# Kernel tuning notes

Hardware: AMD Instinct MI355X
Metric: run time of the kernel (lower is better)

Reference implementation:

```python
import math
import jax, jax.numpy as jnp
from jax import lax
import numpy as np

TWO_PI = 2.0 * math.pi
CG_ITERS = 30      # DifferentiableLinearSolver(max_iter=30)
CG_TOL = 1e-6
CG_REG = 1e-6      # reg = 1e-6 * I added inside the solver


def build_second_diff_matrix(N, dtype):
    e = jnp.ones(N, dtype)
    e2 = -2.0 * e
    e2 = e2.at[0].set(-1.0).at[-1].set(-1.0)
    oper = jnp.diag(e2) + jnp.diag(e[:-1], -1) + jnp.diag(e[:-1], 1)
    return oper.T @ oper


def cumtrapz(y, dx):
    # cumulative trapezoid along last axis, keeping length (leading zero)
    avg = (y[..., :-1] + y[..., 1:]) * (0.5 * dx)
    c = jnp.cumsum(avg, axis=-1)
    return jnp.concatenate([jnp.zeros_like(y[..., :1]), c], axis=-1)


def differ5(y, delta):
    mid = (y[..., 2:] - y[..., :-2]) / (2.0 * delta)
    first = (y[..., 1:2] - y[..., 0:1]) / delta
    last = (y[..., -1:] - y[..., -2:-1]) / delta
    return jnp.concatenate([first, mid, last], axis=-1)


def projec5(vec, var):
    # per-row norm-ball projection; vec: (B, N)
    M = vec.shape[-1]
    e = jnp.sqrt(M * var)
    n = jnp.linalg.norm(vec, axis=-1, keepdims=True)
    scale = jnp.where(n > e, e / jnp.maximum(n, 1e-30), 1.0)
    return vec * scale


def cg_solve(opedoub, coef, diagv, rhs, x0):
    # Solves (coef*opedoub + diag(diagv) + CG_REG*I) x = rhs via CG,
    # matching torch semantics (early break freezes state).
    def mv(p):
        return coef * (opedoub @ p) + (diagv + CG_REG) * p

    r0 = rhs - mv(x0)
    rs0 = jnp.dot(r0, r0)

    def step(carry, _):
        x, r, p, rsold, done = carry
        Ap = mv(p)
        a = rsold / (jnp.dot(p, Ap) + 1e-12)
        x1 = jnp.where(done, x, x + a * p)
        r1 = jnp.where(done, r, r - a * Ap)
        rsnew = jnp.dot(r1, r1)
        done1 = done | (jnp.sqrt(rsnew) < CG_TOL)
        bta = rsnew / (rsold + 1e-12)
        p1 = jnp.where(done1, p, r1 + bta * p)
        rsold1 = jnp.where(done1, rsold, rsnew)
        return (x1, r1, p1, rsold1, done1), None

    (x, _, _, _, _), _ = lax.scan(step, (x0, r0, r0, rs0, jnp.array(False)), None, length=CG_ITERS)
    return x


def _forward(s, eIF, xm, ym, sum_x, sum_y, lamuda, init_freqs, mode_mask,
             alpha, beta, var, fs, iteration,
             fe_w1, fe_b1, fe_w2, fe_b2,
             pr_w1, pr_b1, pr_w2, pr_b2, pr_w3, pr_b3, iter_weight):
    dtype = s.dtype
    B, N = s.shape
    K = eIF.shape[1]

    # ---- hyperparameter refinement MLP ----
    avg = jnp.mean(init_freqs, axis=1, keepdims=True)              # (B,1)
    h = jax.nn.relu(avg @ fe_w1.T + fe_b1)
    h = jax.nn.relu(h @ fe_w2.T + fe_b2)                            # (B,16)
    cur = jnp.stack([jnp.broadcast_to(alpha, (B,)),
                     jnp.broadcast_to(beta, (B,))], axis=1)         # (B,2)
    z = jnp.concatenate([h, cur], axis=1)                           # (B,18)
    z = jax.nn.relu(z @ pr_w1.T + pr_b1)
    z = jax.nn.relu(z @ pr_w2.T + pr_b2)
    res = jnp.tanh(z @ pr_w3.T + pr_b3)                             # (B,2)
    fac = jax.nn.sigmoid(iter_weight * iteration)
    res = res * fac * 0.1
    new_alpha = jnp.clip(alpha + jnp.mean(res[:, 0] * alpha), 1e-6, 0.01)
    new_beta = jnp.clip(beta + jnp.mean(res[:, 1] * beta), 1e-6, 0.1)

    betathr = jnp.minimum(10.0 ** (iteration / 36.0 - 10.0), new_beta)
    opedoub = build_second_diff_matrix(N, dtype)
    dx = 1.0 / fs

    # Within the torch k-loop, temp sums / lamuda / new_eIF[b,k] all still hold
    # their *input* values, so all (b,k) sub-problems are independent -> vmap.
    u = projec5(s - sum_x - sum_y - lamuda / new_alpha, var)        # (B,N)

    phase = TWO_PI * cumtrapz(eIF, dx)                               # (B,K,N)
    cosm = jnp.cos(phase)
    sinm = jnp.sin(phase)
    resid = (s[:, None, :] - (sum_x[:, None, :] - xm * cosm)
             - (sum_y[:, None, :] - ym * sinm)
             - u[:, None, :] - (lamuda / new_alpha)[:, None, :])
    rhs_x = cosm * resid
    rhs_y = sinm * resid

    coefA = 2.0 / new_alpha
    flat = lambda t: t.reshape(B * K, N)
    cg_v = jax.vmap(cg_solve, in_axes=(None, None, 0, 0, 0))

    xs = cg_v(opedoub, coefA, flat(cosm ** 2), flat(rhs_x), flat(xm)).reshape(B, K, N)
    ys = cg_v(opedoub, coefA, flat(sinm ** 2), flat(rhs_y), flat(ym)).reshape(B, K, N)

    xbar = differ5(xs, dx)
    ybar = differ5(ys, dx)
    denom = xs ** 2 + ys ** 2 + 1e-12
    deltaIF = (xs * ybar - ys * xbar) / (denom * TWO_PI)

    coefS = 2.0 / betathr
    ones_d = jnp.ones((B * K, N), dtype)
    zeros_d = jnp.zeros((B * K, N), dtype)
    smooth = cg_v(opedoub, coefS, ones_d, flat(deltaIF), zeros_d).reshape(B, K, N)
    eIF_s = eIF - 0.5 * smooth

    active = (mode_mask != 0)[:, :, None]                            # (B,K,1)
    new_xm = jnp.where(active, xs, xm)
    new_ym = jnp.where(active, ys, ym)
    new_eIF = jnp.where(active, eIF_s, eIF)

    new_phase = TWO_PI * cumtrapz(new_eIF, dx)
    maskf = active.astype(dtype)
    bsx = jnp.sum(maskf * new_xm * jnp.cos(new_phase), axis=1)       # (B,N)
    bsy = jnp.sum(maskf * new_ym * jnp.sin(new_phase), axis=1)
    new_lamuda = lamuda + new_alpha * (u + bsx + bsy - s)

    return (new_eIF, new_xm, new_ym, bsx, bsy, new_lamuda, new_alpha, new_beta)


def setup_inputs() -> dict:
    key = jax.random.key(0)
    B, K, N = 8, 4, 2048
    ks = jax.random.split(key, 20)
    f32 = jnp.float32
    inp = {
        "s": jax.random.normal(ks[0], (B, N), f32),
        "eIF": 50.0 + 200.0 * jax.random.uniform(ks[1], (B, K, N), f32),
        "xm": 0.1 * jax.random.normal(ks[2], (B, K, N), f32),
        "ym": 0.1 * jax.random.normal(ks[3], (B, K, N), f32),
        "sum_x": 0.1 * jax.random.normal(ks[4], (B, N), f32),
        "sum_y": 0.1 * jax.random.normal(ks[5], (B, N), f32),
        "lamuda": 0.01 * jax.random.normal(ks[6], (B, N), f32),
        "init_freqs": 50.0 + 200.0 * jax.random.uniform(ks[7], (B, K), f32),
        "mode_mask": jnp.ones((B, K), jnp.int32),
        "alpha": jnp.asarray(0.005, f32),
        "beta": jnp.asarray(0.05, f32),
        "var": jnp.asarray(0.01, f32),
        "fs": jnp.asarray(2000.0, f32),
        "iteration": 1,
        # HyperparameterRefinement params (torch Linear: y = x @ W.T + b)
        "fe_w1": 0.1 * jax.random.normal(ks[8], (32, 1), f32),
        "fe_b1": jnp.zeros((32,), f32),
        "fe_w2": 0.1 * jax.random.normal(ks[9], (16, 32), f32),
        "fe_b2": jnp.zeros((16,), f32),
        "pr_w1": 0.1 * jax.random.normal(ks[10], (64, 18), f32),
        "pr_b1": jnp.zeros((64,), f32),
        "pr_w2": 0.1 * jax.random.normal(ks[11], (32, 64), f32),
        "pr_b2": jnp.zeros((32,), f32),
        "pr_w3": 0.1 * jax.random.normal(ks[12], (2, 32), f32),
        "pr_b3": jnp.zeros((2,), f32),
        "iter_weight": jnp.asarray(0.1, f32),
    }
    return inp


def reference(s, eIF, xm, ym, sum_x, sum_y, lamuda, init_freqs, mode_mask,
              alpha, beta, var, fs, iteration,
              fe_w1, fe_b1, fe_w2, fe_b2,
              pr_w1, pr_b1, pr_w2, pr_b2, pr_w3, pr_b3, iter_weight):
    return _forward(s, eIF, xm, ym, sum_x, sum_y, lamuda, init_freqs, mode_mask,
                    alpha, beta, var, fs, iteration,
                    fe_w1, fe_b1, fe_w2, fe_b2,
                    pr_w1, pr_b1, pr_w2, pr_b2, pr_w3, pr_b3, iter_weight)
```

## Files before the change

kernel.cpp:

```cpp
#include <hip/hip_runtime.h>
#include <math.h>

#define Nq 2048
#define Bq 8
#define Kq 4
#define BKq 32
#define NL 32
#define TWO_PI_D 6.283185307179586
#define PI_D 3.141592653589793
#define INV2PI_D 0.15915494309189535


__device__ __forceinline__ double wave_sum_d(double v) {
#pragma unroll
  for (int off = 1; off < 64; off <<= 1) v += __shfl_xor(v, off, 64);
  return v;
}

__device__ __forceinline__ float dpp_sum_f32(float v) {
  v += __int_as_float(__builtin_amdgcn_update_dpp(0, __float_as_int(v), 0x111, 0xf, 0xf, false));
  v += __int_as_float(__builtin_amdgcn_update_dpp(0, __float_as_int(v), 0x112, 0xf, 0xf, false));
  v += __int_as_float(__builtin_amdgcn_update_dpp(0, __float_as_int(v), 0x114, 0xf, 0xe, false));
  v += __int_as_float(__builtin_amdgcn_update_dpp(0, __float_as_int(v), 0x118, 0xf, 0xc, false));
  v += __int_as_float(__builtin_amdgcn_update_dpp(0, __float_as_int(v), 0x142, 0xa, 0xf, false));
  v += __int_as_float(__builtin_amdgcn_update_dpp(0, __float_as_int(v), 0x143, 0xc, 0xf, false));
  return __int_as_float(__builtin_amdgcn_readlane(__float_as_int(v), 63));
}

__device__ __forceinline__ float dpp_up1(float v) {
  return __int_as_float(__builtin_amdgcn_update_dpp(0, __float_as_int(v), 0x138, 0xf, 0xf, false));
}
__device__ __forceinline__ float dpp_dn1(float v) {
  return __int_as_float(__builtin_amdgcn_update_dpp(0, __float_as_int(v), 0x130, 0xf, 0xf, false));
}

__device__ __forceinline__ double lane_excl_prefix_d(double T, int lane) {
  double acc = T;
#pragma unroll
  for (int off = 1; off < 64; off <<= 1) {
    double t = __shfl_up(acc, off, 64);
    if (lane >= off) acc += t;
  }
  return acc - T;
}

__device__ __forceinline__ void fast_sincos_ph(double ph, float* sn, float* cs) {
  double k = trunc(ph * INV2PI_D);
  float phr = (float)(ph - k * TWO_PI_D);
  __sincosf(phr, sn, cs);
}

template <bool UNIT>
__device__ __forceinline__ void applyA(const float* p, float* Ap,
                                       const float* dd, float c, float c3,
                                       float c4, float ddu, int lane) {
  float lm1 = dpp_up1(p[NL - 1]);
  float lm2 = dpp_up1(p[NL - 2]);
  float rp1 = dpp_dn1(p[0]);
  float rp2 = dpp_dn1(p[1]);
#pragma unroll
  for (int e = 0; e < NL; ++e) {
    float m2 = (e >= 2) ? p[e - 2] : (e == 1 ? lm1 : lm2);
    float m1 = (e >= 1) ? p[e - 1] : lm1;
    float q1 = (e <= NL - 2) ? p[e + 1] : rp1;
    float q2 = (e <= NL - 3) ? p[e + 2] : (e == NL - 2 ? rp1 : rp2);
    float t1 = m2 + q2, t2 = m1 + q1;
    float u = fmaf(c, t1, -(c4 * t2));
    float d = UNIT ? ddu : dd[e];
    Ap[e] = fmaf(d, p[e], u);
  }
  if (lane == 0) {
    float d0 = (UNIT ? ddu : dd[0]) - c4;
    Ap[0] = fmaf(d0, p[0], fmaf(c, p[2], -(c3 * p[1])));
    float d1 = UNIT ? ddu : dd[1];
    Ap[1] = fmaf(d1, p[1], -(c3 * p[0])) + fmaf(c, p[3], -(c4 * p[2]));
  }
  if (lane == 63) {
    float dm2 = UNIT ? ddu : dd[NL - 2];
    Ap[NL - 2] = fmaf(dm2, p[NL - 2], c * p[NL - 4]) -
                 fmaf(c4, p[NL - 3], c3 * p[NL - 1]);
    float dm1 = (UNIT ? ddu : dd[NL - 1]) - c4;
    Ap[NL - 1] = fmaf(dm1, p[NL - 1], c * p[NL - 3]) - c3 * p[NL - 2];
  }
}

template <bool UNIT>
__device__ __forceinline__ void cg_wave_f(float coef, float* dd, float* r,
                                          float* x, int lane) {
  const float c = coef, c3 = 3.0f * coef, c4 = 4.0f * coef;
  const float ddu = 6.0f * coef + (1.0f + 1e-6f);
  if (!UNIT) {
#pragma unroll
    for (int e = 0; e < NL; ++e) dd[e] += 6.0f * coef;
  }
  float p[NL], Ap[NL];
  applyA<UNIT>(x, Ap, dd, c, c3, c4, ddu, lane);
  float s0 = 0, s1 = 0, s2 = 0, s3 = 0;
#pragma unroll
  for (int e = 0; e < NL; ++e) {
    r[e] -= Ap[e];
    p[e] = r[e];
    float* acc = (e & 2) ? ((e & 1) ? &s3 : &s2) : ((e & 1) ? &s1 : &s0);
    *acc = fmaf(r[e], r[e], *acc);
  }
  float rsold = dpp_sum_f32((s0 + s1) + (s2 + s3));
  for (int it = 0; it < 30; ++it) {
    applyA<UNIT>(p, Ap, dd, c, c3, c4, ddu, lane);
    float d0 = 0, d1 = 0, d2 = 0, d3 = 0;
#pragma unroll
    for (int e = 0; e < NL; ++e) {
      float* acc = (e & 2) ? ((e & 1) ? &d3 : &d2) : ((e & 1) ? &d1 : &d0);
      *acc = fmaf(p[e], Ap[e], *acc);
    }
    float pap = dpp_sum_f32((d0 + d1) + (d2 + d3));
    float a = __fdividef(rsold, pap + 1e-12f);
    float t0 = 0, t1 = 0, t2 = 0, t3 = 0;
#pragma unroll
    for (int e = 0; e < NL; ++e) {
      x[e] = fmaf(a, p[e], x[e]);
      r[e] = fmaf(-a, Ap[e], r[e]);
      float* acc = (e & 2) ? ((e & 1) ? &t3 : &t2) : ((e & 1) ? &t1 : &t0);
      *acc = fmaf(r[e], r[e], *acc);
    }
    float rsnew = dpp_sum_f32((t0 + t1) + (t2 + t3));
    if (rsnew < 1e-12f) break;
    float bta = __fdividef(rsnew, rsold + 1e-12f);
#pragma unroll
    for (int e = 0; e < NL; ++e) p[e] = fmaf(bta, p[e], r[e]);
    rsold = rsnew;
  }
}

__device__ __forceinline__ double blk_reduce(double v, double* sh) {
#pragma unroll
  for (int off = 32; off > 0; off >>= 1) v += __shfl_down(v, off, 64);
  int wid = threadIdx.x >> 6;
  int lane = threadIdx.x & 63;
  __syncthreads();
  if (lane == 0) sh[wid] = v;
  __syncthreads();
  double r = sh[0] + sh[1] + sh[2] + sh[3];
  __syncthreads();
  return r;
}

__global__ __launch_bounds__(128, 1) void row_kernel(
    const float* __restrict__ s, const float* __restrict__ eIF,
    const float* __restrict__ xm, const float* __restrict__ ym,
    const float* __restrict__ sum_x, const float* __restrict__ sum_y,
    const float* __restrict__ lamuda, const float* __restrict__ init_freqs,
    const int* __restrict__ mode_mask, const float* __restrict__ alpha_p,
    const float* __restrict__ beta_p, const float* __restrict__ var_p,
    const float* __restrict__ fs_p, const int* __restrict__ iter_p,
    const float* __restrict__ fe_w1, const float* __restrict__ fe_b1,
    const float* __restrict__ fe_w2, const float* __restrict__ fe_b2,
    const float* __restrict__ pr_w1, const float* __restrict__ pr_b1,
    const float* __restrict__ pr_w2, const float* __restrict__ pr_b2,
    const float* __restrict__ pr_w3, const float* __restrict__ pr_b3,
    const float* __restrict__ iter_w_p, double* __restrict__ hdr,
    float* __restrict__ out_eIF, float* __restrict__ out_xm,
    float* __restrict__ out_ym, float* __restrict__ cx_w,
    float* __restrict__ cy_w, float* __restrict__ out_scal) {
  __shared__ double sh_avg[Bq];
  __shared__ double sh_h1[Bq][32];
  __shared__ double sh_z[Bq][18];
  __shared__ double sh_z1[Bq][64];
  __shared__ double sh_z2[Bq][32];
  __shared__ double sh_res[Bq][2];
  __shared__ double sh_hdr[6];
  __shared__ float sh_xs[Nq], sh_ys[Nq];

  const int tid = threadIdx.x;
  const int wv = tid >> 6, lane = tid & 63;
  const int row = blockIdx.x, b = row >> 2;
  const int bb = b * Nq, base = row * Nq;

  double alpha = (double)alpha_p[0], beta = (double)beta_p[0];
  double iterv = (double)iter_p[0];
  if (tid < Bq) {
    double avg = 0.0;
#pragma unroll
    for (int k = 0; k < Kq; ++k) avg += (double)init_freqs[tid * Kq + k];
    sh_avg[tid] = avg * (1.0 / Kq);
  }
  __syncthreads();
  for (int n = tid; n < 256; n += 128) {
    int b2 = n >> 5, j = n & 31;
    double v = (double)fe_w1[j] * sh_avg[b2] + (double)fe_b1[j];
    sh_h1[b2][j] = v > 0.0 ? v : 0.0;
  }
  __syncthreads();
  {
    int b2 = tid >> 4, j = tid & 15;
    double acc = (double)fe_b2[j];
    for (int i = 0; i < 32; ++i) acc += (double)fe_w2[j * 32 + i] * sh_h1[b2][i];
    sh_z[b2][j] = acc > 0.0 ? acc : 0.0;
  }
  if (tid < Bq) {
    sh_z[tid][16] = alpha;
    sh_z[tid][17] = beta;
  }
  __syncthreads();
  for (int n = tid; n < 512; n += 128) {
    int b2 = n >> 6, j = n & 63;
    double acc = (double)pr_b1[j];
    for (int i = 0; i < 18; ++i) acc += (double)pr_w1[j * 18 + i] * sh_z[b2][i];
    sh_z1[b2][j] = acc > 0.0 ? acc : 0.0;
  }
  __syncthreads();
  for (int n = tid; n < 256; n += 128) {
    int b2 = n >> 5, j = n & 31;
    double acc = (double)pr_b2[j];
    for (int i = 0; i < 64; ++i) acc += (double)pr_w2[j * 64 + i] * sh_z1[b2][i];
    sh_z2[b2][j] = acc > 0.0 ? acc : 0.0;
  }
  __syncthreads();
  if (tid < 16) {
    int b2 = tid >> 1, c = tid & 1;
    double acc = (double)pr_b3[c];
    for (int i = 0; i < 32; ++i) acc += (double)pr_w3[c * 32 + i] * sh_z2[b2][i];
    double fac = 1.0 / (1.0 + exp(-(double)iter_w_p[0] * iterv));
    sh_res[b2][c] = tanh(acc) * fac * 0.1;
  }
  __syncthreads();
  if (tid == 0) {
    double r0 = 0.0, r1 = 0.0;
    for (int q = 0; q < Bq; ++q) { r0 += sh_res[q][0]; r1 += sh_res[q][1]; }
    double na = fmin(fmax(alpha + r0 * alpha * (1.0 / Bq), 1e-6), 0.01);
    double nb = fmin(fmax(beta + r1 * beta * (1.0 / Bq), 1e-6), 0.1);
    double betathr = fmin(pow(10.0, iterv / 36.0 - 10.0), nb);
    sh_hdr[0] = na;
    sh_hdr[1] = 2.0 / na;
    sh_hdr[2] = 2.0 / betathr;
    sh_hdr[3] = 1.0 / na;
    hdr[0] = na;
    hdr[4] = 1.0 / na;
    out_scal[0] = (float)na;
    out_scal[1] = (float)nb;
  }
  __syncthreads();
  const float coefA = (float)sh_hdr[1];
  const float coefS = (float)sh_hdr[2];
  const double inva = sh_hdr[3];

  double tv[NL];
  {
    double n0 = 0.0, n1 = 0.0;
#pragma unroll
    for (int e = 0; e < NL; ++e) {
      int gi = bb + lane * NL + e;
      tv[e] = (double)s[gi] - (double)sum_x[gi] - (double)sum_y[gi] -
              (double)lamuda[gi] * inva;
      ((e & 1) ? n1 : n0) += tv[e] * tv[e];
    }
    double nsq = wave_sum_d(n0 + n1);
    double nn = sqrt(nsq);
    double ee = sqrt((double)Nq * (double)var_p[0]);
    double scale = (nn > ee) ? ee / fmax(nn, 1e-30) : 1.0;
    double oms = 1.0 - scale;
#pragma unroll
    for (int e = 0; e < NL; ++e) tv[e] *= oms;
  }

  const double dx = 1.0 / (double)fs_p[0];
  const double c0 = PI_D * dx;
  float df[NL], r[NL], x[NL];
  {
    double ev[NL], pl[NL];
#pragma unroll
    for (int e = 0; e < NL; ++e) ev[e] = (double)eIF[base + lane * NL + e];
    pl[0] = ev[0];
#pragma unroll
    for (int e = 1; e < NL; ++e) pl[e] = pl[e - 1] + ev[e];
    double offs = lane_excl_prefix_d(pl[NL - 1], lane);
    double y0 = __shfl(ev[0], 0, 64);
#pragma unroll
    for (int e = 0; e < NL; ++e) {
      int i = lane * NL + e;
      double ph = c0 * (2.0 * (offs + pl[e]) - ev[e] - y0);
      float sn, cs;
      fast_sincos_ph(ph, &sn, &cs);
      float xmv = xm[base + i], ymv = ym[base + i];
      double resid = tv[e] + (double)xmv * (double)cs + (double)ymv * (double)sn;
      if (wv == 0) {
        df[e] = cs * cs + 1e-6f;
        r[e] = (float)((double)cs * resid);
        x[e] = xmv;
      } else {
        df[e] = sn * sn + 1e-6f;
        r[e] = (float)((double)sn * resid);
        x[e] = ymv;
      }
    }
  }

  cg_wave_f<false>(coefA, df, r, x, lane);

  {
    float* dst = (wv == 0) ? sh_xs : sh_ys;
#pragma unroll
    for (int e = 0; e < NL; ++e) dst[e * 64 + lane] = x[e];
  }
  __syncthreads();

  {
    float xs[NL], ys[NL];
#pragma unroll
    for (int e = 0; e < NL; ++e) {
      xs[e] = sh_xs[e * 64 + lane];
      ys[e] = sh_ys[e * 64 + lane];
    }
    float invdx = (float)fs_p[0], inv2dx = 0.5f * invdx;
    float xl = __shfl_up(xs[NL - 1], 1, 64), xr = __shfl_down(xs[0], 1, 64);
    float yl = __shfl_up(ys[NL - 1], 1, 64), yr = __shfl_down(ys[0], 1, 64);
#pragma unroll
    for (int e = 0; e < NL; ++e) {
      int i = lane * NL + e;
      float xm1 = (e >= 1) ? xs[e - 1] : xl;
      float xp1 = (e <= NL - 2) ? xs[e + 1] : xr;
      float ym1 = (e >= 1) ? ys[e - 1] : yl;
      float yp1 = (e <= NL - 2) ? ys[e + 1] : yr;
      float xb, yb;
      if (i == 0) {
        xb = (xp1 - xs[e]) * invdx;
        yb = (yp1 - ys[e]) * invdx;
      } else if (i == Nq - 1) {
        xb = (xs[e] - xm1) * invdx;
        yb = (ys[e] - ym1) * invdx;
      } else {
        xb = (xp1 - xm1) * inv2dx;
        yb = (yp1 - ym1) * inv2dx;
      }
      float denom = xs[e] * xs[e] + ys[e] * ys[e] + 1e-12f;
      r[e] = (xs[e] * yb - ys[e] * xb) / (denom * (float)TWO_PI_D);
      x[e] = 0.0f;
    }
  }

  cg_wave_f<true>(coefS, nullptr, r, x, lane);

  bool active = mode_mask[row] != 0;
  double eifn[NL], pl[NL];
#pragma unroll
  for (int e = 0; e < NL; ++e) {
    int i = base + lane * NL + e;
    double eifv = (double)eIF[i];
    eifn[e] = active ? (eifv - 0.5 * (double)x[e]) : eifv;
  }
  if (wv == 0) {
#pragma unroll
    for (int e = 0; e < NL; ++e) {
      int i = base + lane * NL + e;
      out_eIF[i] = (float)eifn[e];
      out_xm[i] = active ? sh_xs[e * 64 + lane] : xm[i];
    }
  } else {
#pragma unroll
    for (int e = 0; e < NL; ++e) {
      int i = base + lane * NL + e;
      out_ym[i] = active ? sh_ys[e * 64 + lane] : ym[i];
    }
  }
  pl[0] = eifn[0];
#pragma unroll
  for (int e = 1; e < NL; ++e) pl[e] = pl[e - 1] + eifn[e];
  double offs = lane_excl_prefix_d(pl[NL - 1], lane);
  double y0 = __shfl(eifn[0], 0, 64);
#pragma unroll
  for (int e = 0; e < NL; ++e) {
    int i = base + lane * NL + e;
    double ph = c0 * (2.0 * (offs + pl[e]) - eifn[e] - y0);
    float sn, cs;
    fast_sincos_ph(ph, &sn, &cs);
    if (wv == 0)
      cx_w[i] = active ? sh_xs[e * 64 + lane] * cs : 0.0f;
    else
      cy_w[i] = active ? sh_ys[e * 64 + lane] * sn : 0.0f;
  }
}

__global__ __launch_bounds__(256) void final_kernel(
    const float* __restrict__ s, const float* __restrict__ sum_x,
    const float* __restrict__ sum_y, const float* __restrict__ lamuda,
    const float* __restrict__ var_p, const double* __restrict__ hdr,
    const float* __restrict__ cx_w, const float* __restrict__ cy_w,
    float* __restrict__ out_bsx, float* __restrict__ out_bsy,
    float* __restrict__ out_lam) {
  __shared__ double sh_red[4];
  __shared__ double sh_scale;
  int b = blockIdx.x;
  int bb = b * Nq;
  int tid = threadIdx.x;
  double na = hdr[0], inva = hdr[4];
  double t[8];
  double loc = 0.0;
#pragma unroll
  for (int e = 0; e < 8; ++e) {
    int gi = bb + tid + e * 256;
    t[e] = (double)s[gi] - (double)sum_x[gi] - (double)sum_y[gi] -
           (double)lamuda[gi] * inva;
    loc += t[e] * t[e];
  }
  double nsq = blk_reduce(loc, sh_red);
  if (tid == 0) {
    double n = sqrt(nsq);
    double ee = sqrt((double)Nq * (double)var_p[0]);
    sh_scale = (n > ee) ? ee / fmax(n, 1e-30) : 1.0;
  }
  __syncthreads();
  double scale = sh_scale;
#pragma unroll
  for (int e = 0; e < 8; ++e) {
    int i = tid + e * 256;
    int gi = bb + i;
    double bx = 0.0, by = 0.0;
#pragma unroll
    for (int k = 0; k < Kq; ++k) {
      bx += (double)cx_w[(b * Kq + k) * Nq + i];
      by += (double)cy_w[(b * Kq + k) * Nq + i];
    }
    double u = t[e] * scale;
    double nl = (double)lamuda[gi] + na * (u + bx + by - (double)s[gi]);
    out_bsx[gi] = (float)bx;
    out_bsy[gi] = (float)by;
    out_lam[gi] = (float)nl;
  }
}

extern "C" void kernel_launch(void* const* d_in, const int* in_sizes, int n_in,
                              void* d_out, int out_size, void* d_ws, size_t ws_size,
                              hipStream_t stream) {
  (void)in_sizes; (void)n_in; (void)out_size; (void)ws_size;
  const float* s = (const float*)d_in[0];
  const float* eIF = (const float*)d_in[1];
  const float* xm = (const float*)d_in[2];
  const float* ym = (const float*)d_in[3];
  const float* sum_x = (const float*)d_in[4];
  const float* sum_y = (const float*)d_in[5];
  const float* lamuda = (const float*)d_in[6];
  const float* init_freqs = (const float*)d_in[7];
  const int* mode_mask = (const int*)d_in[8];
  const float* alpha = (const float*)d_in[9];
  const float* beta = (const float*)d_in[10];
  const float* var = (const float*)d_in[11];
  const float* fs = (const float*)d_in[12];
  const int* iteration = (const int*)d_in[13];
  const float* fe_w1 = (const float*)d_in[14];
  const float* fe_b1 = (const float*)d_in[15];
  const float* fe_w2 = (const float*)d_in[16];
  const float* fe_b2 = (const float*)d_in[17];
  const float* pr_w1 = (const float*)d_in[18];
  const float* pr_b1 = (const float*)d_in[19];
  const float* pr_w2 = (const float*)d_in[20];
  const float* pr_b2 = (const float*)d_in[21];
  const float* pr_w3 = (const float*)d_in[22];
  const float* pr_b3 = (const float*)d_in[23];
  const float* iter_weight = (const float*)d_in[24];

  float* out = (float*)d_out;
  const int BN = Bq * Nq;
  const int BKN = BKq * Nq;
  float* out_eIF = out;
  float* out_xm = out + BKN;
  float* out_ym = out + 2 * BKN;
  float* out_bsx = out + 3 * BKN;
  float* out_bsy = out + 3 * BKN + BN;
  float* out_lam = out + 3 * BKN + 2 * BN;
  float* out_scal = out + 3 * BKN + 3 * BN;

  double* W = (double*)d_ws;
  double* hdr = W;
  float* F = (float*)(W + 16);
  float* cx_w = F;
  float* cy_w = F + BKN;

  row_kernel<<<BKq, 128, 0, stream>>>(
      s, eIF, xm, ym, sum_x, sum_y, lamuda, init_freqs, mode_mask, alpha, beta,
      var, fs, iteration, fe_w1, fe_b1, fe_w2, fe_b2, pr_w1, pr_b1, pr_w2,
      pr_b2, pr_w3, pr_b3, iter_weight, hdr, out_eIF, out_xm, out_ym, cx_w,
      cy_w, out_scal);
  final_kernel<<<Bq, 256, 0, stream>>>(s, sum_x, sum_y, lamuda, var, hdr, cx_w,
                                       cy_w, out_bsx, out_bsy, out_lam);
}
```

Baseline: 172.3 us.

## Split each CG system across two waves with LDS halo and fused dot-product reductions

Each row's two CG solves previously ran on one wave with 32 elements per lane. Now each system is split across two waves of 16 elements per lane, so the block grows to 256 threads. The waves exchange boundary halo values and partial dot products through LDS with __syncthreads each iteration. The residual norm is derived algebraically from p·Ap, Ap·Ap and r·Ap so one barrier serves all reductions. This halves the serial per-wave work on the latency-bound CG, at the cost of extra block barriers per iteration and a less exact float rsnew, since it no longer comes from a direct sum of squared residuals.

New measurement: 173.7 us. No clear change (+0.8%).

```diff
diff --git a/kernel.cpp b/kernel.cpp
--- a/kernel.cpp
+++ b/kernel.cpp
@@ -5,7 +5,7 @@
 #define Bq 8
 #define Kq 4
 #define BKq 32
-#define NL 32
+#define NE 16
 #define TWO_PI_D 6.283185307179586
 #define PI_D 3.141592653589793
 #define INV2PI_D 0.15915494309189535
@@ -51,83 +51,136 @@
 }
 
 template <bool UNIT>
-__device__ __forceinline__ void applyA(const float* p, float* Ap,
-                                       const float* dd, float c, float c3,
-                                       float c4, float ddu, int lane) {
-  float lm1 = dpp_up1(p[NL - 1]);
-  float lm2 = dpp_up1(p[NL - 2]);
+__device__ __forceinline__ void applyA16(const float* p, float* Ap,
+                                         const float* dd, float c, float c3,
+                                         float c4, float ddu, float hL0,
+                                         float hL1, float hR0, float hR1,
+                                         int lane, int half) {
+  float lm1 = dpp_up1(p[NE - 1]);
+  float lm2 = dpp_up1(p[NE - 2]);
   float rp1 = dpp_dn1(p[0]);
   float rp2 = dpp_dn1(p[1]);
-#pragma unroll
-  for (int e = 0; e < NL; ++e) {
+  if (lane == 0) { lm1 = hL1; lm2 = hL0; }
+  if (lane == 63) { rp1 = hR0; rp2 = hR1; }
+#pragma unroll
+  for (int e = 0; e < NE; ++e) {
     float m2 = (e >= 2) ? p[e - 2] : (e == 1 ? lm1 : lm2);
     float m1 = (e >= 1) ? p[e - 1] : lm1;
-    float q1 = (e <= NL - 2) ? p[e + 1] : rp1;
-    float q2 = (e <= NL - 3) ? p[e + 2] : (e == NL - 2 ? rp1 : rp2);
-    float t1 = m2 + q2, t2 = m1 + q1;
-    float u = fmaf(c, t1, -(c4 * t2));
-    float d = UNIT ? ddu : dd[e];
-    Ap[e] = fmaf(d, p[e], u);
-  }
-  if (lane == 0) {
+    float q1 = (e <= NE - 2) ? p[e + 1] : rp1;
+    float q2 = (e <= NE - 3) ? p[e + 2] : (e == NE - 2 ? rp1 : rp2);
+    float u = fmaf(c, m2 + q2, -(c4 * (m1 + q1)));
+    Ap[e] = fmaf(UNIT ? ddu : dd[e], p[e], u);
+  }
+  if (half == 0 && lane == 0) {
     float d0 = (UNIT ? ddu : dd[0]) - c4;
     Ap[0] = fmaf(d0, p[0], fmaf(c, p[2], -(c3 * p[1])));
     float d1 = UNIT ? ddu : dd[1];
     Ap[1] = fmaf(d1, p[1], -(c3 * p[0])) + fmaf(c, p[3], -(c4 * p[2]));
   }
-  if (lane == 63) {
-    float dm2 = UNIT ? ddu : dd[NL - 2];
-    Ap[NL - 2] = fmaf(dm2, p[NL - 2], c * p[NL - 4]) -
-                 fmaf(c4, p[NL - 3], c3 * p[NL - 1]);
-    float dm1 = (UNIT ? ddu : dd[NL - 1]) - c4;
-    Ap[NL - 1] = fmaf(dm1, p[NL - 1], c * p[NL - 3]) - c3 * p[NL - 2];
+  if (half == 1 && lane == 63) {
+    float dm2 = UNIT ? ddu : dd[NE - 2];
+    Ap[NE - 2] = fmaf(dm2, p[NE - 2], c * p[NE - 4]) -
+                 fmaf(c4, p[NE - 3], c3 * p[NE - 1]);
+    float dm1 = (UNIT ? ddu : dd[NE - 1]) - c4;
+    Ap[NE - 1] = fmaf(dm1, p[NE - 1], c * p[NE - 3]) - c3 * p[NE - 2];
   }
 }
 
 template <bool UNIT>
-__device__ __forceinline__ void cg_wave_f(float coef, float* dd, float* r,
-                                          float* x, int lane) {
+__device__ __forceinline__ void cg_wave2(float coef, float* dd, float* r,
+                                         float* x, float hxL0, float hxL1,
+                                         float hxR0, float hxR1, int lane,
+                                         int half, int wv,
+                                         float (*sh_part)[4],
+                                         float (*sh_rb)[2]) {
   const float c = coef, c3 = 3.0f * coef, c4 = 4.0f * coef;
   const float ddu = 6.0f * coef + (1.0f + 1e-6f);
   if (!UNIT) {
 #pragma unroll
-    for (int e = 0; e < NL; ++e) dd[e] += 6.0f * coef;
-  }
-  float p[NL], Ap[NL];
-  applyA<UNIT>(x, Ap, dd, c, c3, c4, ddu, lane);
-  float s0 = 0, s1 = 0, s2 = 0, s3 = 0;
-#pragma unroll
-  for (int e = 0; e < NL; ++e) {
+    for (int e = 0; e < NE; ++e) dd[e] += 6.0f * coef;
+  }
+  const int nb = wv ^ 1;
+  float p[NE], Ap[NE];
+  applyA16<UNIT>(x, Ap, dd, c, c3, c4, ddu, hxL0, hxL1, hxR0, hxR1, lane, half);
+  float s0 = 0.f, s1 = 0.f;
+#pragma unroll
+  for (int e = 0; e < NE; ++e) {
     r[e] -= Ap[e];
     p[e] = r[e];
-    float* acc = (e & 2) ? ((e & 1) ? &s3 : &s2) : ((e & 1) ? &s1 : &s0);
-    *acc = fmaf(r[e], r[e], *acc);
-  }
-  float rsold = dpp_sum_f32((s0 + s1) + (s2 + s3));
+    ((e & 1) ? s1 : s0) = fmaf(r[e], r[e], (e & 1) ? s1 : s0);
+  }
+  float rsp = dpp_sum_f32(s0 + s1);
+  if (lane == 0) sh_part[wv][3] = rsp;
+  if (half == 0) {
+    if (lane == 63) { sh_rb[wv][0] = r[NE - 2]; sh_rb[wv][1] = r[NE - 1]; }
+  } else {
+    if (lane == 0) { sh_rb[wv][0] = r[0]; sh_rb[wv][1] = r[1]; }
+  }
+  __syncthreads();
+  float rs = rsp + sh_part[nb][3];
+  float hL0 = 0.f, hL1 = 0.f, hR0 = 0.f, hR1 = 0.f;
+  if (half == 1) { hL0 = sh_rb[nb][0]; hL1 = sh_rb[nb][1]; }
+  else { hR0 = sh_rb[nb][0]; hR1 = sh_rb[nb][1]; }
+  bool done = false;
   for (int it = 0; it < 30; ++it) {
-    applyA<UNIT>(p, Ap, dd, c, c3, c4, ddu, lane);
-    float d0 = 0, d1 = 0, d2 = 0, d3 = 0;
-#pragma unroll
-    for (int e = 0; e < NL; ++e) {
-      float* acc = (e & 2) ? ((e & 1) ? &d3 : &d2) : ((e & 1) ? &d1 : &d0);
-      *acc = fmaf(p[e], Ap[e], *acc);
-    }
-    float pap = dpp_sum_f32((d0 + d1) + (d2 + d3));
-    float a = __fdividef(rsold, pap + 1e-12f);
-    float t0 = 0, t1 = 0, t2 = 0, t3 = 0;
-#pragma unroll
-    for (int e = 0; e < NL; ++e) {
-      x[e] = fmaf(a, p[e], x[e]);
-      r[e] = fmaf(-a, Ap[e], r[e]);
-      float* acc = (e & 2) ? ((e & 1) ? &t3 : &t2) : ((e & 1) ? &t1 : &t0);
-      *acc = fmaf(r[e], r[e], *acc);
-    }
-    float rsnew = dpp_sum_f32((t0 + t1) + (t2 + t3));
-    if (rsnew < 1e-12f) break;
-    float bta = __fdividef(rsnew, rsold + 1e-12f);
-#pragma unroll
-    for (int e = 0; e < NL; ++e) p[e] = fmaf(bta, p[e], r[e]);
-    rsold = rsnew;
+    applyA16<UNIT>(p, Ap, dd, c, c3, c4, ddu, hL0, hL1, hR0, hR1, lane, half);
+    float pa0 = 0.f, pa1 = 0.f, aa0 = 0.f, aa1 = 0.f, ra0 = 0.f, ra1 = 0.f;
+#pragma unroll
+    for (int e = 0; e < NE; ++e) {
+      if (e & 1) {
+        pa1 = fmaf(p[e], Ap[e], pa1);
+        aa1 = fmaf(Ap[e], Ap[e], aa1);
+        ra1 = fmaf(r[e], Ap[e], ra1);
+      } else {
+        pa0 = fmaf(p[e], Ap[e], pa0);
+        aa0 = fmaf(Ap[e], Ap[e], aa0);
+        ra0 = fmaf(r[e], Ap[e], ra0);
+      }
+    }
+    float papp = dpp_sum_f32(pa0 + pa1);
+    float aapp = dpp_sum_f32(aa0 + aa1);
+    float rapp = dpp_sum_f32(ra0 + ra1);
+    if (lane == 0) {
+      sh_part[wv][0] = papp;
+      sh_part[wv][1] = aapp;
+      sh_part[wv][2] = rapp;
+    }
+    __syncthreads();
+    float pap = papp + sh_part[nb][0];
+    float apap = aapp + sh_part[nb][1];
+    float rap = rapp + sh_part[nb][2];
+    float a = __fdividef(rs, pap + 1e-12f);
+    float rsnew = fmaf(a * a, apap, fmaf(-2.0f * a, rap, rs));
+    if (!done) {
+#pragma unroll
+      for (int e = 0; e < NE; ++e) {
+        x[e] = fmaf(a, p[e], x[e]);
+        r[e] = fmaf(-a, Ap[e], r[e]);
+      }
+    }
+    bool done1 = done || (rsnew < 1e-12f);
+    float bta = __fdividef(rsnew, rs + 1e-12f);
+    if (!done1) {
+#pragma unroll
+      for (int e = 0; e < NE; ++e) p[e] = fmaf(bta, p[e], r[e]);
+      rs = rsnew;
+      if (half == 0) {
+        if (lane == 63) { sh_rb[wv][0] = r[NE - 2]; sh_rb[wv][1] = r[NE - 1]; }
+      } else {
+        if (lane == 0) { sh_rb[wv][0] = r[0]; sh_rb[wv][1] = r[1]; }
+      }
+    }
+    __syncthreads();
+    if (!done1) {
+      if (half == 1) {
+        hL0 = fmaf(bta, hL0, sh_rb[nb][0]);
+        hL1 = fmaf(bta, hL1, sh_rb[nb][1]);
+      } else {
+        hR0 = fmaf(bta, hR0, sh_rb[nb][0]);
+        hR1 = fmaf(bta, hR1, sh_rb[nb][1]);
+      }
+    }
+    done = done1;
   }
 }
 
@@ -144,7 +197,7 @@
   return r;
 }
 
-__global__ __launch_bounds__(128, 1) void row_kernel(
+__global__ __launch_bounds__(256, 1) void row_kernel(
     const float* __restrict__ s, const float* __restrict__ eIF,
     const float* __restrict__ xm, const float* __restrict__ ym,
     const float* __restrict__ sum_x, const float* __restrict__ sum_y,
@@ -167,13 +220,18 @@
   __shared__ double sh_z1[Bq][64];
   __shared__ double sh_z2[Bq][32];
   __shared__ double sh_res[Bq][2];
-  __shared__ double sh_hdr[6];
+  __shared__ double sh_hdr[4];
+  __shared__ double sh_sc[8];
+  __shared__ float sh_part[4][4];
+  __shared__ float sh_rb[4][2];
   __shared__ float sh_xs[Nq], sh_ys[Nq];
 
   const int tid = threadIdx.x;
   const int wv = tid >> 6, lane = tid & 63;
+  const int pair = wv >> 1, half = wv & 1;
   const int row = blockIdx.x, b = row >> 2;
   const int bb = b * Nq, base = row * Nq;
+  const int seg0 = half * 1024;
 
   double alpha = (double)alpha_p[0], beta = (double)beta_p[0];
   double iterv = (double)iter_p[0];
@@ -184,32 +242,32 @@
     sh_avg[tid] = avg * (1.0 / Kq);
   }
   __syncthreads();
-  for (int n = tid; n < 256; n += 128) {
-    int b2 = n >> 5, j = n & 31;
+  {
+    int b2 = tid >> 5, j = tid & 31;
     double v = (double)fe_w1[j] * sh_avg[b2] + (double)fe_b1[j];
     sh_h1[b2][j] = v > 0.0 ? v : 0.0;
   }
   __syncthreads();
-  {
+  if (tid < 128) {
     int b2 = tid >> 4, j = tid & 15;
     double acc = (double)fe_b2[j];
     for (int i = 0; i < 32; ++i) acc += (double)fe_w2[j * 32 + i] * sh_h1[b2][i];
     sh_z[b2][j] = acc > 0.0 ? acc : 0.0;
   }
-  if (tid < Bq) {
-    sh_z[tid][16] = alpha;
-    sh_z[tid][17] = beta;
-  }
-  __syncthreads();
-  for (int n = tid; n < 512; n += 128) {
+  if (tid >= 128 && tid < 128 + Bq) {
+    sh_z[tid - 128][16] = alpha;
+    sh_z[tid - 128][17] = beta;
+  }
+  __syncthreads();
+  for (int n = tid; n < 512; n += 256) {
     int b2 = n >> 6, j = n & 63;
     double acc = (double)pr_b1[j];
     for (int i = 0; i < 18; ++i) acc += (double)pr_w1[j * 18 + i] * sh_z[b2][i];
     sh_z1[b2][j] = acc > 0.0 ? acc : 0.0;
   }
   __syncthreads();
-  for (int n = tid; n < 256; n += 128) {
-    int b2 = n >> 5, j = n & 31;
+  {
+    int b2 = tid >> 5, j = tid & 31;
     double acc = (double)pr_b2[j];
     for (int i = 0; i < 64; ++i) acc += (double)pr_w2[j * 64 + i] * sh_z1[b2][i];
     sh_z2[b2][j] = acc > 0.0 ? acc : 0.0;
@@ -227,8 +285,8 @@
     double r0 = 0.0, r1 = 0.0;
     for (int q = 0; q < Bq; ++q) { r0 += sh_res[q][0]; r1 += sh_res[q][1]; }
     double na = fmin(fmax(alpha + r0 * alpha * (1.0 / Bq), 1e-6), 0.01);
-    double nb = fmin(fmax(beta + r1 * beta * (1.0 / Bq), 1e-6), 0.1);
-    double betathr = fmin(pow(10.0, iterv / 36.0 - 10.0), nb);
+    double nb2 = fmin(fmax(beta + r1 * beta * (1.0 / Bq), 1e-6), 0.1);
+    double betathr = fmin(pow(10.0, iterv / 36.0 - 10.0), nb2);
     sh_hdr[0] = na;
     sh_hdr[1] = 2.0 / na;
     sh_hdr[2] = 2.0 / betathr;
@@ -236,146 +294,161 @@
     hdr[0] = na;
     hdr[4] = 1.0 / na;
     out_scal[0] = (float)na;
-    out_scal[1] = (float)nb;
+    out_scal[1] = (float)nb2;
   }
   __syncthreads();
   const float coefA = (float)sh_hdr[1];
   const float coefS = (float)sh_hdr[2];
   const double inva = sh_hdr[3];
 
-  double tv[NL];
-  {
-    double n0 = 0.0, n1 = 0.0;
-#pragma unroll
-    for (int e = 0; e < NL; ++e) {
-      int gi = bb + lane * NL + e;
+  double tv[NE];
+  {
+    double n0 = 0.0;
+#pragma unroll
+    for (int e = 0; e < NE; ++e) {
+      int gi = bb + seg0 + lane * NE + e;
       tv[e] = (double)s[gi] - (double)sum_x[gi] - (double)sum_y[gi] -
               (double)lamuda[gi] * inva;
-      ((e & 1) ? n1 : n0) += tv[e] * tv[e];
-    }
-    double nsq = wave_sum_d(n0 + n1);
+      n0 += tv[e] * tv[e];
+    }
+    double np = wave_sum_d(n0);
+    if (pair == 0 && lane == 0) sh_sc[4 + half] = np;
+  }
+  const double dx = 1.0 / (double)fs_p[0];
+  const double c0 = PI_D * dx;
+  double ev[NE], pl[NE];
+#pragma unroll
+  for (int e = 0; e < NE; ++e) ev[e] = (double)eIF[base + seg0 + lane * NE + e];
+  pl[0] = ev[0];
+#pragma unroll
+  for (int e = 1; e < NE; ++e) pl[e] = pl[e - 1] + ev[e];
+  double offs_w = lane_excl_prefix_d(pl[NE - 1], lane);
+  {
+    double segT = __shfl(offs_w + pl[NE - 1], 63, 64);
+    if (pair == 0 && lane == 0) sh_sc[half] = segT;
+    if (pair == 0 && half == 0 && lane == 0) sh_sc[2] = ev[0];
+  }
+  __syncthreads();
+  double offs = offs_w + (half ? sh_sc[0] : 0.0);
+  double y0 = sh_sc[2];
+  {
+    double nsq = sh_sc[4] + sh_sc[5];
     double nn = sqrt(nsq);
     double ee = sqrt((double)Nq * (double)var_p[0]);
     double scale = (nn > ee) ? ee / fmax(nn, 1e-30) : 1.0;
     double oms = 1.0 - scale;
 #pragma unroll
-    for (int e = 0; e < NL; ++e) tv[e] *= oms;
-  }
-
-  const double dx = 1.0 / (double)fs_p[0];
-  const double c0 = PI_D * dx;
-  float df[NL], r[NL], x[NL];
-  {
-    double ev[NL], pl[NL];
-#pragma unroll
-    for (int e = 0; e < NL; ++e) ev[e] = (double)eIF[base + lane * NL + e];
-    pl[0] = ev[0];
-#pragma unroll
-    for (int e = 1; e < NL; ++e) pl[e] = pl[e - 1] + ev[e];
-    double offs = lane_excl_prefix_d(pl[NL - 1], lane);
-    double y0 = __shfl(ev[0], 0, 64);
-#pragma unroll
-    for (int e = 0; e < NL; ++e) {
-      int i = lane * NL + e;
-      double ph = c0 * (2.0 * (offs + pl[e]) - ev[e] - y0);
+    for (int e = 0; e < NE; ++e) tv[e] *= oms;
+  }
+
+  float dd[NE], r[NE], x[NE];
+#pragma unroll
+  for (int e = 0; e < NE; ++e) {
+    int i = seg0 + lane * NE + e;
+    double ph = c0 * (2.0 * (offs + pl[e]) - ev[e] - y0);
+    float sn, cs;
+    fast_sincos_ph(ph, &sn, &cs);
+    float xmv = xm[base + i], ymv = ym[base + i];
+    double resid = tv[e] + (double)xmv * (double)cs + (double)ymv * (double)sn;
+    if (pair == 0) {
+      dd[e] = cs * cs + 1e-6f;
+      r[e] = (float)((double)cs * resid);
+      x[e] = xmv;
+    } else {
+      dd[e] = sn * sn + 1e-6f;
+      r[e] = (float)((double)sn * resid);
+      x[e] = ymv;
+    }
+  }
+  {
+    const float* src = (pair == 0) ? (xm + base) : (ym + base);
+    float hxL0 = 0.f, hxL1 = 0.f, hxR0 = 0.f, hxR1 = 0.f;
+    if (half == 0) { hxR0 = src[1024]; hxR1 = src[1025]; }
+    else { hxL0 = src[1022]; hxL1 = src[1023]; }
+    cg_wave2<false>(coefA, dd, r, x, hxL0, hxL1, hxR0, hxR1, lane, half, wv,
+                    sh_part, sh_rb);
+  }
+
+  {
+    float* dst = (pair == 0) ? sh_xs : sh_ys;
+#pragma unroll
+    for (int e = 0; e < NE; ++e) dst[seg0 + lane * NE + e] = x[e];
+  }
+  __syncthreads();
+
+  {
+    float invdx = (float)fs_p[0], inv2dx = 0.5f * invdx;
+#pragma unroll
+    for (int e = 0; e < NE; ++e) {
+      int i = seg0 + lane * NE + e;
+      float xc = sh_xs[i], yc = sh_ys[i];
+      float xb, yb;
+      if (i == 0) {
+        xb = (sh_xs[1] - sh_xs[0]) * invdx;
+        yb = (sh_ys[1] - sh_ys[0]) * invdx;
+      } else if (i == Nq - 1) {
+        xb = (sh_xs[Nq - 1] - sh_xs[Nq - 2]) * invdx;
+        yb = (sh_ys[Nq - 1] - sh_ys[Nq - 2]) * invdx;
+      } else {
+        xb = (sh_xs[i + 1] - sh_xs[i - 1]) * inv2dx;
+        yb = (sh_ys[i + 1] - sh_ys[i - 1]) * inv2dx;
+      }
+      float denom = xc * xc + yc * yc + 1e-12f;
+      r[e] = (xc * yb - yc * xb) / (denom * (float)TWO_PI_D);
+      x[e] = 0.0f;
+    }
+  }
+  __syncthreads();
+
+  cg_wave2<true>(coefS, nullptr, r, x, 0.f, 0.f, 0.f, 0.f, lane, half, wv,
+                 sh_part, sh_rb);
+
+  bool active = mode_mask[row] != 0;
+  double eifn[NE];
+#pragma unroll
+  for (int e = 0; e < NE; ++e) {
+    int i = seg0 + lane * NE + e;
+    double eifv = (double)eIF[base + i];
+    eifn[e] = active ? (eifv - 0.5 * (double)x[e]) : eifv;
+  }
+  if (pair == 0) {
+#pragma unroll
+    for (int e = 0; e < NE; ++e) {
+      int i = seg0 + lane * NE + e;
+      out_eIF[base + i] = (float)eifn[e];
+      out_xm[base + i] = active ? sh_xs[i] : xm[base + i];
+    }
+  } else {
+#pragma unroll
+    for (int e = 0; e < NE; ++e) {
+      int i = seg0 + lane * NE + e;
+      out_ym[base + i] = active ? sh_ys[i] : ym[base + i];
+    }
+  }
+  pl[0] = eifn[0];
+#pragma unroll
+  for (int e = 1; e < NE; ++e) pl[e] = pl[e - 1] + eifn[e];
+  offs_w = lane_excl_prefix_d(pl[NE - 1], lane);
+  {
+    double segT = __shfl(offs_w + pl[NE - 1], 63, 64);
+    if (pair == 0 && half == 0 && lane == 0) sh_sc[6] = segT;
+    if (pair == 0 && half == 0 && lane == 0) sh_sc[3] = eifn[0];
+  }
+  __syncthreads();
+  {
+    double offs2 = offs_w + (half ? sh_sc[6] : 0.0);
+    double y02 = sh_sc[3];
+#pragma unroll
+    for (int e = 0; e < NE; ++e) {
+      int i = seg0 + lane * NE + e;
+      double ph = c0 * (2.0 * (offs2 + pl[e]) - eifn[e] - y02);
       float sn, cs;
       fast_sincos_ph(ph, &sn, &cs);
-      float xmv = xm[base + i], ymv = ym[base + i];
-      double resid = tv[e] + (double)xmv * (double)cs + (double)ymv * (double)sn;
-      if (wv == 0) {
-        df[e] = cs * cs + 1e-6f;
-        r[e] = (float)((double)cs * resid);
-        x[e] = xmv;
-      } else {
-        df[e] = sn * sn + 1e-6f;
-        r[e] = (float)((double)sn * resid);
-        x[e] = ymv;
-      }
-    }
-  }
-
-  cg_wave_f<false>(coefA, df, r, x, lane);
-
-  {
-    float* dst = (wv == 0) ? sh_xs : sh_ys;
-#pragma unroll
-    for (int e = 0; e < NL; ++e) dst[e * 64 + lane] = x[e];
-  }
-  __syncthreads();
-
-  {
-    float xs[NL], ys[NL];
-#pragma unroll
-    for (int e = 0; e < NL; ++e) {
-      xs[e] = sh_xs[e * 64 + lane];
-      ys[e] = sh_ys[e * 64 + lane];
-    }
-    float invdx = (float)fs_p[0], inv2dx = 0.5f * invdx;
-    float xl = __shfl_up(xs[NL - 1], 1, 64), xr = __shfl_down(xs[0], 1, 64);
-    float yl = __shfl_up(ys[NL - 1], 1, 64), yr = __shfl_down(ys[0], 1, 64);
-#pragma unroll
-    for (int e = 0; e < NL; ++e) {
-      int i = lane * NL + e;
-      float xm1 = (e >= 1) ? xs[e - 1] : xl;
-      float xp1 = (e <= NL - 2) ? xs[e + 1] : xr;
-      float ym1 = (e >= 1) ? ys[e - 1] : yl;
-      float yp1 = (e <= NL - 2) ? ys[e + 1] : yr;
-      float xb, yb;
-      if (i == 0) {
-        xb = (xp1 - xs[e]) * invdx;
-        yb = (yp1 - ys[e]) * invdx;
-      } else if (i == Nq - 1) {
-        xb = (xs[e] - xm1) * invdx;
-        yb = (ys[e] - ym1) * invdx;
-      } else {
-        xb = (xp1 - xm1) * inv2dx;
-        yb = (yp1 - ym1) * inv2dx;
-      }
-      float denom = xs[e] * xs[e] + ys[e] * ys[e] + 1e-12f;
-      r[e] = (xs[e] * yb - ys[e] * xb) / (denom * (float)TWO_PI_D);
-      x[e] = 0.0f;
-    }
-  }
-
-  cg_wave_f<true>(coefS, nullptr, r, x, lane);
-
-  bool active = mode_mask[row] != 0;
-  double eifn[NL], pl[NL];
-#pragma unroll
-  for (int e = 0; e < NL; ++e) {
-    int i = base + lane * NL + e;
-    double eifv = (double)eIF[i];
-    eifn[e] = active ? (eifv - 0.5 * (double)x[e]) : eifv;
-  }
-  if (wv == 0) {
-#pragma unroll
-    for (int e = 0; e < NL; ++e) {
-      int i = base + lane * NL + e;
-      out_eIF[i] = (float)eifn[e];
-      out_xm[i] = active ? sh_xs[e * 64 + lane] : xm[i];
-    }
-  } else {
-#pragma unroll
-    for (int e = 0; e < NL; ++e) {
-      int i = base + lane * NL + e;
-      out_ym[i] = active ? sh_ys[e * 64 + lane] : ym[i];
-    }
-  }
-  pl[0] = eifn[0];
-#pragma unroll
-  for (int e = 1; e < NL; ++e) pl[e] = pl[e - 1] + eifn[e];
-  double offs = lane_excl_prefix_d(pl[NL - 1], lane);
-  double y0 = __shfl(eifn[0], 0, 64);
-#pragma unroll
-  for (int e = 0; e < NL; ++e) {
-    int i = base + lane * NL + e;
-    double ph = c0 * (2.0 * (offs + pl[e]) - eifn[e] - y0);
-    float sn, cs;
-    fast_sincos_ph(ph, &sn, &cs);
-    if (wv == 0)
-      cx_w[i] = active ? sh_xs[e * 64 + lane] * cs : 0.0f;
-    else
-      cy_w[i] = active ? sh_ys[e * 64 + lane] * sn : 0.0f;
+      if (pair == 0)
+        cx_w[base + i] = active ? sh_xs[i] * cs : 0.0f;
+      else
+        cy_w[base + i] = active ? sh_ys[i] * sn : 0.0f;
+    }
   }
 }
 
@@ -474,7 +547,7 @@
   float* cx_w = F;
   float* cy_w = F + BKN;
 
-  row_kernel<<<BKq, 128, 0, stream>>>(
+  row_kernel<<<BKq, 256, 0, stream>>>(
       s, eIF, xm, ym, sum_x, sum_y, lamuda, init_freqs, mode_mask, alpha, beta,
       var, fs, iteration, fe_w1, fe_b1, fe_w2, fe_b2, pr_w1, pr_b1, pr_w2,
       pr_b2, pr_w3, pr_b3, iter_weight, hdr, out_eIF, out_xm, out_ym, cx_w,
```
